# Kernel tuning notes

Hardware: AMD Instinct MI355X
Metric: run time of the kernel (lower is better)

Reference implementation:

```python
import jax, jax.numpy as jnp
import numpy as np

N_USERS, N_MOVIES, N_EDGES = 100000, 20000, 1000000
IN_UNITS, NUM_CLASSES = 128, 5


def _xavier(key, shape):
    # torch xavier_uniform_ on a Linear weight [out, in]; we store transposed [in, out]
    fan_in, fan_out = shape[0], shape[1]
    a = jnp.sqrt(6.0 / (fan_in + fan_out))
    return jax.random.uniform(key, shape, dtype=jnp.float32, minval=-a, maxval=a)


def setup_inputs() -> dict:
    key = jax.random.key(0)
    k1, k2, k3, k4, k5, k6, k7 = jax.random.split(key, 7)
    ufeat = jax.random.normal(k1, (N_USERS, IN_UNITS), dtype=jnp.float32)
    ifeat = jax.random.normal(k2, (N_MOVIES, IN_UNITS), dtype=jnp.float32)
    src_idx = jax.random.randint(k3, (N_EDGES,), 0, N_USERS, dtype=jnp.int32)
    dst_idx = jax.random.randint(k4, (N_EDGES,), 0, N_MOVIES, dtype=jnp.int32)
    W1 = _xavier(k5, (2 * IN_UNITS, IN_UNITS))   # Linear(2*in_units -> in_units)
    W2 = _xavier(k6, (IN_UNITS, IN_UNITS))       # Linear(in_units -> in_units)
    Wp = _xavier(k7, (IN_UNITS, NUM_CLASSES))    # predictor Linear(in_units -> num_classes)
    return {"ufeat": ufeat, "ifeat": ifeat, "src_idx": src_idx, "dst_idx": dst_idx,
            "W1": W1, "W2": W2, "Wp": Wp}


def reference(ufeat, ifeat, W1, W2, Wp, src_idx, dst_idx):
    # gather per-edge src/dst node features
    h_u = ufeat[src_idx]                 # [E, D]
    h_v = ifeat[dst_idx]                 # [E, D]
    h = jnp.concatenate([h_u, h_v], axis=1)          # [E, 2D]
    h = jax.nn.gelu(h @ W1, approximate=False)        # [E, D] (torch GELU default = exact erf)
    h = h @ W2                                        # [E, D]
    score = h @ Wp                                    # [E, C]
    return jnp.squeeze(score)
```

## Files before the change

kernel.cpp:

```cpp
#include <hip/hip_runtime.h>
#include <hip/hip_bf16.h>

#define D 128

typedef short bf16x8 __attribute__((ext_vector_type(8)));
typedef float f32x4 __attribute__((ext_vector_type(4)));
typedef float f32x2 __attribute__((ext_vector_type(2)));

__device__ __forceinline__ unsigned short f2bf(float x) {
    __hip_bfloat16 h = __float2bfloat16(x);
    return *reinterpret_cast<unsigned short*>(&h);
}
__device__ __forceinline__ float bflo(unsigned int w) { return __uint_as_float(w << 16); }
__device__ __forceinline__ float bfhi(unsigned int w) { return __uint_as_float(w & 0xffff0000u); }

__device__ __forceinline__ f32x2 gelu2(f32x2 z) {
    f32x2 z2 = z * z;
    f32x2 c1 = {0.1029466f, 0.1029466f};
    f32x2 c0 = {2.3022646f, 2.3022646f};
    f32x2 xe = z * __builtin_elementwise_fma(z2, c1, c0);
    f32x2 q;
    q.x = __builtin_amdgcn_exp2f(xe.x);
    q.y = __builtin_amdgcn_exp2f(xe.y);
    f32x2 d = q + 1.0f;
    f32x2 r;
    r.x = __builtin_amdgcn_rcpf(d.x);
    r.y = __builtin_amdgcn_rcpf(d.y);
    return __builtin_elementwise_fma(-z, r, z);
}

__device__ __forceinline__ float gelu_erf(float z) {
    float y = fabsf(z) * 0.70710678118654752f;
    float t = __builtin_amdgcn_rcpf(1.0f + 0.3275911f * y);
    float poly = ((((1.061405429f * t - 1.453152027f) * t + 1.421413741f) * t
                   - 0.284496736f) * t + 0.254829592f) * t;
    float e = __expf(-y * y);
    float erfv = 1.0f - poly * e;
    erfv = copysignf(erfv, z);
    return 0.5f * z * (1.0f + erfv);
}

__device__ __forceinline__ void node_body(const float* __restrict__ feat,
                                          const float* __restrict__ W1,
                                          int base_k, int Nn, int blk,
                                          unsigned short* __restrict__ outbf) {
    __shared__ unsigned short sB[128 * 136];
    const int t = threadIdx.x;
    const int r0 = blk * 64;

    #pragma unroll
    for (int i = 0; i < 16; ++i) {
        int f = (i * 256 + t) * 4;
        int k = f >> 7, j = f & 127;
        float4 v = *reinterpret_cast<const float4*>(&W1[(size_t)(base_k + k) * D + j]);
        sB[(j + 0) * 136 + k] = f2bf(v.x);
        sB[(j + 1) * 136 + k] = f2bf(v.y);
        sB[(j + 2) * 136 + k] = f2bf(v.z);
        sB[(j + 3) * 136 + k] = f2bf(v.w);
    }
    __syncthreads();

    const int wid = t >> 6, l = t & 63;
    const int m16 = l & 15, g4 = l >> 4;
    const int arow = r0 + wid * 16 + m16;
    const bool rok = arow < Nn;
    const float* rp = feat + (size_t)(rok ? arow : 0) * D;

    f32x4 acc[8];
    #pragma unroll
    for (int n = 0; n < 8; ++n) acc[n] = (f32x4){0.f, 0.f, 0.f, 0.f};

    #pragma unroll
    for (int kk = 0; kk < 4; ++kk) {
        int k0 = kk * 32 + g4 * 8;
        float4 f0 = make_float4(0.f, 0.f, 0.f, 0.f), f1 = f0;
        if (rok) {
            f0 = *reinterpret_cast<const float4*>(rp + k0);
            f1 = *reinterpret_cast<const float4*>(rp + k0 + 4);
        }
        union { bf16x8 v; unsigned short u[8]; } a;
        a.u[0] = f2bf(f0.x); a.u[1] = f2bf(f0.y); a.u[2] = f2bf(f0.z); a.u[3] = f2bf(f0.w);
        a.u[4] = f2bf(f1.x); a.u[5] = f2bf(f1.y); a.u[6] = f2bf(f1.z); a.u[7] = f2bf(f1.w);
        #pragma unroll
        for (int n = 0; n < 8; ++n) {
            bf16x8 b = *reinterpret_cast<const bf16x8*>(&sB[(n * 16 + m16) * 136 + k0]);
            acc[n] = __builtin_amdgcn_mfma_f32_16x16x32_bf16(a.v, b, acc[n], 0, 0, 0);
        }
    }
    #pragma unroll
    for (int n = 0; n < 8; ++n) {
        #pragma unroll
        for (int r = 0; r < 4; ++r) {
            int row = r0 + wid * 16 + g4 * 4 + r;
            if (row < Nn) outbf[(size_t)row * D + n * 16 + m16] = f2bf(acc[n][r]);
        }
    }
}

__global__ __launch_bounds__(256) void prep_kernel(const float* __restrict__ uf,
                                                   const float* __restrict__ vf,
                                                   const float* __restrict__ W1,
                                                   const float* __restrict__ W2,
                                                   const float* __restrict__ Wp,
                                                   int NU, int NM, int nbU, int nbM,
                                                   unsigned short* __restrict__ Abf,
                                                   unsigned short* __restrict__ Bbf,
                                                   unsigned short* __restrict__ Wcbf) {
    int b = blockIdx.x;
    if (b < nbU) {
        node_body(uf, W1, 0, NU, b, Abf);
    } else if (b < nbU + nbM) {
        node_body(vf, W1, D, NM, b - nbU, Bbf);
    } else {
        int t = threadIdx.x;
        #pragma unroll
        for (int i = 0; i < 8; ++i) {
            int idx = i * 256 + t;
            int col = idx >> 7, k = idx & 127;
            float acc = 0.f;
            if (col < 5) {
                #pragma unroll 8
                for (int j = 0; j < D; ++j) acc += W2[k * D + j] * Wp[j * 5 + col];
            }
            Wcbf[col * D + k] = f2bf(acc);
        }
    }
}

__global__ __launch_bounds__(256, 4) void edge_kernel(const unsigned short* __restrict__ A,
                                                      const unsigned short* __restrict__ B,
                                                      const int* __restrict__ src,
                                                      const int* __restrict__ dst,
                                                      const unsigned short* __restrict__ Wcbf,
                                                      float* __restrict__ out, int E) {
    const int l    = threadIdx.x & 63;
    const int er   = l & 15;
    const int quad = l >> 4;
    const int wid  = blockIdx.x * 4 + (threadIdx.x >> 6);
    const int nw   = gridDim.x * 4;

    bf16x8 wfrag[4];
    #pragma unroll
    for (int kk = 0; kk < 4; ++kk)
        wfrag[kk] = *reinterpret_cast<const bf16x8*>(&Wcbf[er * D + kk * 32 + quad * 8]);

    const int P = (E + 31) >> 5;
    if (wid >= P) return;
    const int Emax = E - 1;

    int ia = wid * 32 + er, ib = ia + 16;
    int sa = src[min(ia, Emax)], da = dst[min(ia, Emax)];
    int sb = src[min(ib, Emax)], db = dst[min(ib, Emax)];

    for (int p = wid; p < P; p += nw) {
        int pn = p + nw;
        int pc = pn < P ? pn : p;
        int ja = pc * 32 + er, jb = ja + 16;
        int san = src[min(ja, Emax)], dan = dst[min(ja, Emax)];
        int sbn = src[min(jb, Emax)], dbn = dst[min(jb, Emax)];

        const unsigned short* apA = A + ((size_t)sa << 7) + quad * 8;
        const unsigned short* bpA = B + ((size_t)da << 7) + quad * 8;
        const unsigned short* apB = A + ((size_t)sb << 7) + quad * 8;
        const unsigned short* bpB = B + ((size_t)db << 7) + quad * 8;
        uint4 a0[4], b0[4], a1[4], b1[4];
        #pragma unroll
        for (int kk = 0; kk < 4; ++kk) {
            a0[kk] = *reinterpret_cast<const uint4*>(apA + kk * 32);
            b0[kk] = *reinterpret_cast<const uint4*>(bpA + kk * 32);
            a1[kk] = *reinterpret_cast<const uint4*>(apB + kk * 32);
            b1[kk] = *reinterpret_cast<const uint4*>(bpB + kk * 32);
        }

        f32x4 accA = (f32x4){0.f, 0.f, 0.f, 0.f};
        f32x4 accB = accA;
        #pragma unroll
        for (int kk = 0; kk < 4; ++kk) {
            unsigned int aw[4] = {a0[kk].x, a0[kk].y, a0[kk].z, a0[kk].w};
            unsigned int bw[4] = {b0[kk].x, b0[kk].y, b0[kk].z, b0[kk].w};
            union { bf16x8 v; unsigned short u[8]; } frag;
            #pragma unroll
            for (int pp = 0; pp < 4; ++pp) {
                f32x2 za = {bflo(aw[pp]), bfhi(aw[pp])};
                f32x2 zb = {bflo(bw[pp]), bfhi(bw[pp])};
                f32x2 g = gelu2(za + zb);
                frag.u[2 * pp]     = f2bf(g.x);
                frag.u[2 * pp + 1] = f2bf(g.y);
            }
            accA = __builtin_amdgcn_mfma_f32_16x16x32_bf16(frag.v, wfrag[kk], accA, 0, 0, 0);
        }
        #pragma unroll
        for (int kk = 0; kk < 4; ++kk) {
            unsigned int aw[4] = {a1[kk].x, a1[kk].y, a1[kk].z, a1[kk].w};
            unsigned int bw[4] = {b1[kk].x, b1[kk].y, b1[kk].z, b1[kk].w};
            union { bf16x8 v; unsigned short u[8]; } frag;
            #pragma unroll
            for (int pp = 0; pp < 4; ++pp) {
                f32x2 za = {bflo(aw[pp]), bfhi(aw[pp])};
                f32x2 zb = {bflo(bw[pp]), bfhi(bw[pp])};
                f32x2 g = gelu2(za + zb);
                frag.u[2 * pp]     = f2bf(g.x);
                frag.u[2 * pp + 1] = f2bf(g.y);
            }
            accB = __builtin_amdgcn_mfma_f32_16x16x32_bf16(frag.v, wfrag[kk], accB, 0, 0, 0);
        }

        int e0 = p << 5;
        #pragma unroll
        for (int r = 0; r < 4; ++r) {
            int eA = e0 + quad * 4 + r;
            if (er < 5 && eA < E) out[(size_t)eA * 5 + er] = accA[r];
        }
        #pragma unroll
        for (int r = 0; r < 4; ++r) {
            int eB = e0 + 16 + quad * 4 + r;
            if (er < 5 && eB < E) out[(size_t)eB * 5 + er] = accB[r];
        }
        sa = san; da = dan; sb = sbn; db = dbn;
    }
}

__global__ __launch_bounds__(256) void fused_fallback(const float* __restrict__ uf,
                                                      const float* __restrict__ vf,
                                                      const int* __restrict__ src,
                                                      const int* __restrict__ dst,
                                                      const float* __restrict__ W1,
                                                      const float* __restrict__ W2,
                                                      const float* __restrict__ Wp,
                                                      float* __restrict__ out, int E) {
    __shared__ unsigned short sW[256 * 128];
    __shared__ float sWc[5 * 128];
    __shared__ float sH[4][256];
    const int t = threadIdx.x;
    #pragma unroll
    for (int i = 0; i < 32; ++i) {
        int f = (i * 256 + t) * 4;
        float4 v = *reinterpret_cast<const float4*>(&W1[f]);
        sW[f + 0] = f2bf(v.x); sW[f + 1] = f2bf(v.y);
        sW[f + 2] = f2bf(v.z); sW[f + 3] = f2bf(v.w);
    }
    for (int idx = t; idx < 640; idx += 256) {
        int c = idx >> 7, k = idx & 127;
        float a = 0.f;
        for (int m = 0; m < 128; ++m) a += W2[k * 128 + m] * Wp[m * 5 + c];
        sWc[c * 128 + k] = a;
    }
    __syncthreads();
    const int wid = t >> 6, l = t & 63;
    const int nw = gridDim.x * 4;
    for (int e = blockIdx.x * 4 + wid; e < E; e += nw) {
        int s = src[e], d0 = dst[e];
        float2 hu = *reinterpret_cast<const float2*>(&uf[(size_t)s * 128 + 2 * l]);
        float2 hv = *reinterpret_cast<const float2*>(&vf[(size_t)d0 * 128 + 2 * l]);
        sH[wid][2 * l] = hu.x; sH[wid][2 * l + 1] = hu.y;
        sH[wid][128 + 2 * l] = hv.x; sH[wid][128 + 2 * l + 1] = hv.y;
        __builtin_amdgcn_wave_barrier();
        float z0 = 0.f, z1 = 0.f;
        for (int k = 0; k < 256; ++k) {
            float h = sH[wid][k];
            z0 += h * __uint_as_float((unsigned int)sW[k * 128 + l] << 16);
            z1 += h * __uint_as_float((unsigned int)sW[k * 128 + l + 64] << 16);
        }
        float g0 = gelu_erf(z0), g1 = gelu_erf(z1);
        float acc[5];
        #pragma unroll
        for (int c = 0; c < 5; ++c)
            acc[c] = g0 * sWc[c * 128 + l] + g1 * sWc[c * 128 + l + 64];
        #pragma unroll
        for (int c = 0; c < 5; ++c) {
            float v = acc[c];
            v += __shfl_xor(v, 1);  v += __shfl_xor(v, 2);
            v += __shfl_xor(v, 4);  v += __shfl_xor(v, 8);
            v += __shfl_xor(v, 16); v += __shfl_xor(v, 32);
            acc[c] = v;
        }
        float v = acc[0];
        if (l == 1) v = acc[1];
        if (l == 2) v = acc[2];
        if (l == 3) v = acc[3];
        if (l == 4) v = acc[4];
        if (l < 5) out[(size_t)e * 5 + l] = v;
        __builtin_amdgcn_wave_barrier();
    }
}

extern "C" void kernel_launch(void* const* d_in, const int* in_sizes, int n_in,
                              void* d_out, int out_size, void* d_ws, size_t ws_size,
                              hipStream_t stream) {
    const float* ufeat = (const float*)d_in[0];
    const float* ifeat = (const float*)d_in[1];
    const int*   src   = (const int*)d_in[2];
    const int*   dst   = (const int*)d_in[3];
    const float* W1    = (const float*)d_in[4];
    const float* W2    = (const float*)d_in[5];
    const float* Wp    = (const float*)d_in[6];
    float* out = (float*)d_out;

    const int NU = in_sizes[0] / D;
    const int NM = in_sizes[1] / D;
    const int E  = in_sizes[2];

    size_t off_A = 4096;
    size_t szA = (size_t)NU * D * 2;
    size_t off_B = off_A + ((szA + 255) / 256) * 256;
    size_t need = off_B + (size_t)NM * D * 2;

    if (ws_size >= need) {
        unsigned short* Wcbf = (unsigned short*)d_ws;
        unsigned short* Abf  = (unsigned short*)((char*)d_ws + off_A);
        unsigned short* Bbf  = (unsigned short*)((char*)d_ws + off_B);
        int nbU = (NU + 63) / 64, nbM = (NM + 63) / 64;
        prep_kernel<<<dim3(nbU + nbM + 1), dim3(256), 0, stream>>>(
            ufeat, ifeat, W1, W2, Wp, NU, NM, nbU, nbM, Abf, Bbf, Wcbf);
        int P = (E + 31) >> 5;
        int blocks = (P + 3) / 4; if (blocks > 2048) blocks = 2048;
        edge_kernel<<<dim3(blocks), dim3(256), 0, stream>>>(Abf, Bbf, src, dst, Wcbf, out, E);
    } else {
        fused_fallback<<<dim3(4096), dim3(256), 0, stream>>>(ufeat, ifeat, src, dst,
                                                             W1, W2, Wp, out, E);
    }
}
```

Measured before the change: 113.9 us.

## Split weight prep, stream W1 from global in node GEMM, double-buffer edge gathers

Node projection now runs one 16-row tile per wave. It reads a bf16 transposed W1 built once by a small prep kernel, instead of having every block transpose W1 into LDS. The edge kernel moves from 32-edge pairs to 16-edge groups with explicit ping-pong prefetch, so the next group's row gathers and index loads are issued before the current group is computed. Index loads and output stores use nontemporal hints, and the edge grid is fixed at 1024 blocks. This adds a third kernel launch and relies on L2/L1 to serve the W1 fragments that were previously held in LDS.

```diff
diff --git a/kernel.cpp b/kernel.cpp
--- a/kernel.cpp
+++ b/kernel.cpp
@@ -40,79 +40,22 @@
     return 0.5f * z * (1.0f + erfv);
 }
 
-__device__ __forceinline__ void node_body(const float* __restrict__ feat,
-                                          const float* __restrict__ W1,
-                                          int base_k, int Nn, int blk,
-                                          unsigned short* __restrict__ outbf) {
-    __shared__ unsigned short sB[128 * 136];
-    const int t = threadIdx.x;
-    const int r0 = blk * 64;
-
-    #pragma unroll
-    for (int i = 0; i < 16; ++i) {
-        int f = (i * 256 + t) * 4;
-        int k = f >> 7, j = f & 127;
-        float4 v = *reinterpret_cast<const float4*>(&W1[(size_t)(base_k + k) * D + j]);
-        sB[(j + 0) * 136 + k] = f2bf(v.x);
-        sB[(j + 1) * 136 + k] = f2bf(v.y);
-        sB[(j + 2) * 136 + k] = f2bf(v.z);
-        sB[(j + 3) * 136 + k] = f2bf(v.w);
-    }
-    __syncthreads();
-
-    const int wid = t >> 6, l = t & 63;
-    const int m16 = l & 15, g4 = l >> 4;
-    const int arow = r0 + wid * 16 + m16;
-    const bool rok = arow < Nn;
-    const float* rp = feat + (size_t)(rok ? arow : 0) * D;
-
-    f32x4 acc[8];
-    #pragma unroll
-    for (int n = 0; n < 8; ++n) acc[n] = (f32x4){0.f, 0.f, 0.f, 0.f};
-
-    #pragma unroll
-    for (int kk = 0; kk < 4; ++kk) {
-        int k0 = kk * 32 + g4 * 8;
-        float4 f0 = make_float4(0.f, 0.f, 0.f, 0.f), f1 = f0;
-        if (rok) {
-            f0 = *reinterpret_cast<const float4*>(rp + k0);
-            f1 = *reinterpret_cast<const float4*>(rp + k0 + 4);
-        }
-        union { bf16x8 v; unsigned short u[8]; } a;
-        a.u[0] = f2bf(f0.x); a.u[1] = f2bf(f0.y); a.u[2] = f2bf(f0.z); a.u[3] = f2bf(f0.w);
-        a.u[4] = f2bf(f1.x); a.u[5] = f2bf(f1.y); a.u[6] = f2bf(f1.z); a.u[7] = f2bf(f1.w);
-        #pragma unroll
-        for (int n = 0; n < 8; ++n) {
-            bf16x8 b = *reinterpret_cast<const bf16x8*>(&sB[(n * 16 + m16) * 136 + k0]);
-            acc[n] = __builtin_amdgcn_mfma_f32_16x16x32_bf16(a.v, b, acc[n], 0, 0, 0);
-        }
-    }
-    #pragma unroll
-    for (int n = 0; n < 8; ++n) {
-        #pragma unroll
-        for (int r = 0; r < 4; ++r) {
-            int row = r0 + wid * 16 + g4 * 4 + r;
-            if (row < Nn) outbf[(size_t)row * D + n * 16 + m16] = f2bf(acc[n][r]);
-        }
-    }
-}
-
-__global__ __launch_bounds__(256) void prep_kernel(const float* __restrict__ uf,
-                                                   const float* __restrict__ vf,
-                                                   const float* __restrict__ W1,
-                                                   const float* __restrict__ W2,
-                                                   const float* __restrict__ Wp,
-                                                   int NU, int NM, int nbU, int nbM,
-                                                   unsigned short* __restrict__ Abf,
-                                                   unsigned short* __restrict__ Bbf,
-                                                   unsigned short* __restrict__ Wcbf) {
-    int b = blockIdx.x;
-    if (b < nbU) {
-        node_body(uf, W1, 0, NU, b, Abf);
-    } else if (b < nbU + nbM) {
-        node_body(vf, W1, D, NM, b - nbU, Bbf);
+__global__ __launch_bounds__(256) void prep0_kernel(const float* __restrict__ W1,
+                                                    const float* __restrict__ W2,
+                                                    const float* __restrict__ Wp,
+                                                    unsigned short* __restrict__ W1T,
+                                                    unsigned short* __restrict__ Wcbf) {
+    const int b = blockIdx.x, t = threadIdx.x;
+    if (b < 16) {
+        #pragma unroll
+        for (int i = 0; i < 8; ++i) {
+            int row = b * 16 + i * 2 + (t >> 7);
+            int j = t & 127;
+            float v = W1[(size_t)row * D + j];
+            int h = row >> 7, k = row & 127;
+            W1T[(size_t)h * 16384 + j * 128 + k] = f2bf(v);
+        }
     } else {
-        int t = threadIdx.x;
         #pragma unroll
         for (int i = 0; i < 8; ++i) {
             int idx = i * 256 + t;
@@ -124,6 +67,105 @@
             }
             Wcbf[col * D + k] = f2bf(acc);
         }
+    }
+}
+
+__global__ __launch_bounds__(256) void node_kernel(const float* __restrict__ uf,
+                                                   const float* __restrict__ vf,
+                                                   const unsigned short* __restrict__ W1T,
+                                                   int NU, int NM, int wU,
+                                                   unsigned short* __restrict__ Abf,
+                                                   unsigned short* __restrict__ Bbf) {
+    const int wv = blockIdx.x * 4 + (threadIdx.x >> 6);
+    const int l = threadIdx.x & 63;
+    const int m16 = l & 15, g4 = l >> 4;
+
+    const float* feat;
+    unsigned short* outp;
+    int Nn, tile, h;
+    if (wv < wU) { feat = uf; outp = Abf; Nn = NU; tile = wv;      h = 0; }
+    else         { feat = vf; outp = Bbf; Nn = NM; tile = wv - wU; h = 1; }
+    const int r0 = tile * 16;
+    if (r0 >= Nn) return;
+
+    const int arow = r0 + m16;
+    const bool rok = arow < Nn;
+    const float* rp = feat + (size_t)(rok ? arow : 0) * D;
+
+    union { bf16x8 v; unsigned short u[8]; } afr[4];
+    #pragma unroll
+    for (int kk = 0; kk < 4; ++kk) {
+        int k0 = kk * 32 + g4 * 8;
+        float4 f0 = make_float4(0.f, 0.f, 0.f, 0.f), f1 = f0;
+        if (rok) {
+            f0 = *reinterpret_cast<const float4*>(rp + k0);
+            f1 = *reinterpret_cast<const float4*>(rp + k0 + 4);
+        }
+        afr[kk].u[0] = f2bf(f0.x); afr[kk].u[1] = f2bf(f0.y);
+        afr[kk].u[2] = f2bf(f0.z); afr[kk].u[3] = f2bf(f0.w);
+        afr[kk].u[4] = f2bf(f1.x); afr[kk].u[5] = f2bf(f1.y);
+        afr[kk].u[6] = f2bf(f1.z); afr[kk].u[7] = f2bf(f1.w);
+    }
+
+    const unsigned short* wt = W1T + (size_t)h * 16384;
+    f32x4 acc[8];
+    #pragma unroll
+    for (int n = 0; n < 8; ++n) acc[n] = (f32x4){0.f, 0.f, 0.f, 0.f};
+    #pragma unroll
+    for (int n = 0; n < 8; ++n) {
+        #pragma unroll
+        for (int kk = 0; kk < 4; ++kk) {
+            bf16x8 bfr = *reinterpret_cast<const bf16x8*>(
+                wt + ((n * 16 + m16) << 7) + kk * 32 + g4 * 8);
+            acc[n] = __builtin_amdgcn_mfma_f32_16x16x32_bf16(afr[kk].v, bfr, acc[n], 0, 0, 0);
+        }
+    }
+    #pragma unroll
+    for (int n = 0; n < 8; ++n) {
+        #pragma unroll
+        for (int r = 0; r < 4; ++r) {
+            int row = r0 + g4 * 4 + r;
+            if (row < Nn) outp[(size_t)row * D + n * 16 + m16] = f2bf(acc[n][r]);
+        }
+    }
+}
+
+__device__ __forceinline__ void issue8(const unsigned short* __restrict__ A,
+                                       const unsigned short* __restrict__ B,
+                                       int s, int d, int quad, uint4* av, uint4* bv) {
+    const unsigned short* ap = A + ((size_t)s << 7) + quad * 8;
+    const unsigned short* bp = B + ((size_t)d << 7) + quad * 8;
+    #pragma unroll
+    for (int kk = 0; kk < 4; ++kk) {
+        av[kk] = *reinterpret_cast<const uint4*>(ap + kk * 32);
+        bv[kk] = *reinterpret_cast<const uint4*>(bp + kk * 32);
+    }
+}
+
+__device__ __forceinline__ void compute_store(const uint4* av, const uint4* bv,
+                                              const bf16x8* wfrag, float* __restrict__ out,
+                                              int g, int E, int er, int quad) {
+    f32x4 acc = (f32x4){0.f, 0.f, 0.f, 0.f};
+    #pragma unroll
+    for (int kk = 0; kk < 4; ++kk) {
+        unsigned int aw[4] = {av[kk].x, av[kk].y, av[kk].z, av[kk].w};
+        unsigned int bw[4] = {bv[kk].x, bv[kk].y, bv[kk].z, bv[kk].w};
+        union { bf16x8 v; unsigned short u[8]; } frag;
+        #pragma unroll
+        for (int pp = 0; pp < 4; ++pp) {
+            f32x2 za = {bflo(aw[pp]), bfhi(aw[pp])};
+            f32x2 zb = {bflo(bw[pp]), bfhi(bw[pp])};
+            f32x2 gl = gelu2(za + zb);
+            frag.u[2 * pp]     = f2bf(gl.x);
+            frag.u[2 * pp + 1] = f2bf(gl.y);
+        }
+        acc = __builtin_amdgcn_mfma_f32_16x16x32_bf16(frag.v, wfrag[kk], acc, 0, 0, 0);
+    }
+    int e0 = g << 4;
+    #pragma unroll
+    for (int r = 0; r < 4; ++r) {
+        int e = e0 + quad * 4 + r;
+        if (er < 5 && e < E) __builtin_nontemporal_store(acc[r], &out[(size_t)e * 5 + er]);
     }
 }
 
@@ -144,79 +186,41 @@
     for (int kk = 0; kk < 4; ++kk)
         wfrag[kk] = *reinterpret_cast<const bf16x8*>(&Wcbf[er * D + kk * 32 + quad * 8]);
 
-    const int P = (E + 31) >> 5;
-    if (wid >= P) return;
-    const int Emax = E - 1;
-
-    int ia = wid * 32 + er, ib = ia + 16;
-    int sa = src[min(ia, Emax)], da = dst[min(ia, Emax)];
-    int sb = src[min(ib, Emax)], db = dst[min(ib, Emax)];
-
-    for (int p = wid; p < P; p += nw) {
-        int pn = p + nw;
-        int pc = pn < P ? pn : p;
-        int ja = pc * 32 + er, jb = ja + 16;
-        int san = src[min(ja, Emax)], dan = dst[min(ja, Emax)];
-        int sbn = src[min(jb, Emax)], dbn = dst[min(jb, Emax)];
-
-        const unsigned short* apA = A + ((size_t)sa << 7) + quad * 8;
-        const unsigned short* bpA = B + ((size_t)da << 7) + quad * 8;
-        const unsigned short* apB = A + ((size_t)sb << 7) + quad * 8;
-        const unsigned short* bpB = B + ((size_t)db << 7) + quad * 8;
-        uint4 a0[4], b0[4], a1[4], b1[4];
-        #pragma unroll
-        for (int kk = 0; kk < 4; ++kk) {
-            a0[kk] = *reinterpret_cast<const uint4*>(apA + kk * 32);
-            b0[kk] = *reinterpret_cast<const uint4*>(bpA + kk * 32);
-            a1[kk] = *reinterpret_cast<const uint4*>(apB + kk * 32);
-            b1[kk] = *reinterpret_cast<const uint4*>(bpB + kk * 32);
-        }
-
-        f32x4 accA = (f32x4){0.f, 0.f, 0.f, 0.f};
-        f32x4 accB = accA;
-        #pragma unroll
-        for (int kk = 0; kk < 4; ++kk) {
-            unsigned int aw[4] = {a0[kk].x, a0[kk].y, a0[kk].z, a0[kk].w};
-            unsigned int bw[4] = {b0[kk].x, b0[kk].y, b0[kk].z, b0[kk].w};
-            union { bf16x8 v; unsigned short u[8]; } frag;
-            #pragma unroll
-            for (int pp = 0; pp < 4; ++pp) {
-                f32x2 za = {bflo(aw[pp]), bfhi(aw[pp])};
-                f32x2 zb = {bflo(bw[pp]), bfhi(bw[pp])};
-                f32x2 g = gelu2(za + zb);
-                frag.u[2 * pp]     = f2bf(g.x);
-                frag.u[2 * pp + 1] = f2bf(g.y);
-            }
-            accA = __builtin_amdgcn_mfma_f32_16x16x32_bf16(frag.v, wfrag[kk], accA, 0, 0, 0);
-        }
-        #pragma unroll
-        for (int kk = 0; kk < 4; ++kk) {
-            unsigned int aw[4] = {a1[kk].x, a1[kk].y, a1[kk].z, a1[kk].w};
-            unsigned int bw[4] = {b1[kk].x, b1[kk].y, b1[kk].z, b1[kk].w};
-            union { bf16x8 v; unsigned short u[8]; } frag;
-            #pragma unroll
-            for (int pp = 0; pp < 4; ++pp) {
-                f32x2 za = {bflo(aw[pp]), bfhi(aw[pp])};
-                f32x2 zb = {bflo(bw[pp]), bfhi(bw[pp])};
-                f32x2 g = gelu2(za + zb);
-                frag.u[2 * pp]     = f2bf(g.x);
-                frag.u[2 * pp + 1] = f2bf(g.y);
-            }
-            accB = __builtin_amdgcn_mfma_f32_16x16x32_bf16(frag.v, wfrag[kk], accB, 0, 0, 0);
-        }
-
-        int e0 = p << 5;
-        #pragma unroll
-        for (int r = 0; r < 4; ++r) {
-            int eA = e0 + quad * 4 + r;
-            if (er < 5 && eA < E) out[(size_t)eA * 5 + er] = accA[r];
-        }
-        #pragma unroll
-        for (int r = 0; r < 4; ++r) {
-            int eB = e0 + 16 + quad * 4 + r;
-            if (er < 5 && eB < E) out[(size_t)eB * 5 + er] = accB[r];
-        }
-        sa = san; da = dan; sb = sbn; db = dbn;
+    const int G = (E + 15) >> 4;
+    if (wid >= G) return;
+    const int Gm = G - 1;
+
+    uint4 aA[4], bA[4], aB[4], bB[4];
+    int g = wid;
+    {
+        int s0 = __builtin_nontemporal_load(&src[g * 16 + er]);
+        int d0 = __builtin_nontemporal_load(&dst[g * 16 + er]);
+        issue8(A, B, s0, d0, quad, aA, bA);
+    }
+    int gi = (g + nw <= Gm) ? g + nw : g;
+    int sN = __builtin_nontemporal_load(&src[gi * 16 + er]);
+    int dN = __builtin_nontemporal_load(&dst[gi * 16 + er]);
+
+    while (true) {
+        issue8(A, B, sN, dN, quad, aB, bB);
+        {
+            int g2 = g + 2 * nw;
+            int gj = (g2 <= Gm) ? g2 : g;
+            sN = __builtin_nontemporal_load(&src[gj * 16 + er]);
+            dN = __builtin_nontemporal_load(&dst[gj * 16 + er]);
+        }
+        compute_store(aA, bA, wfrag, out, g, E, er, quad);
+        g += nw; if (g > Gm) break;
+
+        issue8(A, B, sN, dN, quad, aA, bA);
+        {
+            int g2 = g + 2 * nw;
+            int gj = (g2 <= Gm) ? g2 : g;
+            sN = __builtin_nontemporal_load(&src[gj * 16 + er]);
+            dN = __builtin_nontemporal_load(&dst[gj * 16 + er]);
+        }
+        compute_store(aB, bB, wfrag, out, g, E, er, quad);
+        g += nw; if (g > Gm) break;
     }
 }
 
@@ -300,21 +304,25 @@
     const int NM = in_sizes[1] / D;
     const int E  = in_sizes[2];
 
-    size_t off_A = 4096;
-    size_t szA = (size_t)NU * D * 2;
-    size_t off_B = off_A + ((szA + 255) / 256) * 256;
-    size_t need = off_B + (size_t)NM * D * 2;
+    size_t off_W1T = 4096;
+    size_t off_A   = off_W1T + 65536;
+    size_t szA     = (size_t)NU * D * 2;
+    size_t off_B   = off_A + ((szA + 255) / 256) * 256;
+    size_t need    = off_B + (size_t)NM * D * 2;
 
     if (ws_size >= need) {
         unsigned short* Wcbf = (unsigned short*)d_ws;
+        unsigned short* W1T  = (unsigned short*)((char*)d_ws + off_W1T);
         unsigned short* Abf  = (unsigned short*)((char*)d_ws + off_A);
         unsigned short* Bbf  = (unsigned short*)((char*)d_ws + off_B);
-        int nbU = (NU + 63) / 64, nbM = (NM + 63) / 64;
-        prep_kernel<<<dim3(nbU + nbM + 1), dim3(256), 0, stream>>>(
-            ufeat, ifeat, W1, W2, Wp, NU, NM, nbU, nbM, Abf, Bbf, Wcbf);
-        int P = (E + 31) >> 5;
-        int blocks = (P + 3) / 4; if (blocks > 2048) blocks = 2048;
-        edge_kernel<<<dim3(blocks), dim3(256), 0, stream>>>(Abf, Bbf, src, dst, Wcbf, out, E);
+
+        prep0_kernel<<<dim3(17), dim3(256), 0, stream>>>(W1, W2, Wp, W1T, Wcbf);
+
+        int wU = (NU + 15) / 16, wV = (NM + 15) / 16;
+        int nblk = (wU + wV + 3) / 4;
+        node_kernel<<<dim3(nblk), dim3(256), 0, stream>>>(ufeat, ifeat, W1T, NU, NM, wU, Abf, Bbf);
+
+        edge_kernel<<<dim3(1024), dim3(256), 0, stream>>>(Abf, Bbf, src, dst, Wcbf, out, E);
     } else {
         fused_fallback<<<dim3(4096), dim3(256), 0, stream>>>(ufeat, ifeat, src, dst,
                                                              W1, W2, Wp, out, E);
```

Result: slower. 137.2 us (+20.4%).
